# Optimization experiments

Hardware: AMD Instinct MI355X
Metric: run time of the kernel (lower is better)

The kernel has to match this reference:

```python
import jax, jax.numpy as jnp
import numpy as np

L, D, H, KS, VS, HID = 2048, 1024, 16, 1024, 1024, 4096
EPS = 1e-5


def _linear_params(key, din, dout):
    # torch nn.Linear default init: U(-1/sqrt(din), 1/sqrt(din))
    s = 1.0 / np.sqrt(din)
    kw, kb = jax.random.split(key)
    W = jax.random.uniform(kw, (dout, din), minval=-s, maxval=s, dtype=jnp.float32)
    b = jax.random.uniform(kb, (dout,), minval=-s, maxval=s, dtype=jnp.float32)
    return W, b


def setup_inputs() -> dict:
    key = jax.random.key(0)
    ks = jax.random.split(key, 12)
    x = jax.random.normal(ks[0], (L, D), dtype=jnp.float32)
    # inverse shortest-path lengths in [0, 1]
    shortest_path = jax.random.uniform(ks[1], (L, L), dtype=jnp.float32)
    Wq, bq = _linear_params(ks[2], D, KS)
    Wk, bk = _linear_params(ks[3], D, KS)
    Wv, bv = _linear_params(ks[4], D, VS)
    Wqp, bqp = _linear_params(ks[5], KS, KS)
    Wkp, bkp = _linear_params(ks[6], KS, KS)
    Wvp, bvp = _linear_params(ks[7], VS, VS)
    Wo, bo = _linear_params(ks[8], VS, D)
    W1, b1 = _linear_params(ks[9], D, HID)
    W2, b2 = _linear_params(ks[10], HID, D)
    g1 = jnp.ones((D,), jnp.float32); be1 = jnp.zeros((D,), jnp.float32)
    g2 = jnp.ones((D,), jnp.float32); be2 = jnp.zeros((D,), jnp.float32)
    return dict(x=x, shortest_path=shortest_path,
                Wq=Wq, bq=bq, Wk=Wk, bk=bk, Wv=Wv, bv=bv,
                Wqp=Wqp, bqp=bqp, Wkp=Wkp, bkp=bkp, Wvp=Wvp, bvp=bvp,
                Wo=Wo, bo=bo, W1=W1, b1=b1, W2=W2, b2=b2,
                g1=g1, be1=be1, g2=g2, be2=be2)


def _dense(h, W, b):
    return h @ W.T + b


def _layernorm(h, g, b):
    mu = jnp.mean(h, axis=-1, keepdims=True)
    var = jnp.mean(jnp.square(h - mu), axis=-1, keepdims=True)
    return (h - mu) * jax.lax.rsqrt(var + EPS) * g + b


def reference(x, shortest_path, Wq, bq, Wk, bk, Wv, bv, Wqp, bqp, Wkp, bkp,
              Wvp, bvp, Wo, bo, W1, b1, W2, b2, g1, be1, g2, be2):
    hd = KS // H
    vhd = VS // H
    q = _dense(_dense(x, Wq, bq), Wqp, bqp).reshape(L, H, hd).transpose(1, 0, 2)   # [H,L,hd]
    k = _dense(_dense(x, Wk, bk), Wkp, bkp).reshape(L, H, hd).transpose(1, 0, 2)   # [H,L,hd]
    v = _dense(_dense(x, Wv, bv), Wvp, bvp).reshape(L, H, vhd).transpose(1, 0, 2)  # [H,L,vhd]
    att = jnp.einsum('hld,hmd->hlm', q, k) / jnp.sqrt(jnp.float32(hd))             # [H,L,L]
    sp_bias = jax.nn.softmax(shortest_path, axis=-1) * 0.5                          # [L,L]
    att = jax.nn.softmax(att + sp_bias[None, :, :], axis=-1)
    o = jnp.einsum('hlm,hmd->hld', att, v).transpose(1, 0, 2).reshape(L, VS)        # [L,VS]
    o = _dense(o, Wo, bo)
    h = _layernorm(x + o, g1, be1)                # residual + LN1 (dropout=identity)
    f = jax.nn.relu(_dense(jax.nn.relu(_dense(h, W1, b1)), W2, b2))
    return _layernorm(h + f, g2, be2)             # residual + LN2
```

## Files before the change

### kernel.cpp

```cpp
#include <hip/hip_runtime.h>

typedef __attribute__((ext_vector_type(4))) float f32x4;
typedef __attribute__((ext_vector_type(8))) short s16x8;

static __device__ __forceinline__ ushort f2b(float f) {
  union { float f; unsigned u; } v; v.f = f;
  unsigned u = v.u;
  unsigned r = (u + 0x7fffu + ((u >> 16) & 1u)) >> 16;
  return (ushort)r;
}
static __device__ __forceinline__ float b2f(ushort h) {
  union { unsigned u; float f; } v; v.u = ((unsigned)h) << 16;
  return v.f;
}

static __device__ __forceinline__ void gload_lds16(const ushort* g, ushort* l) {
  __builtin_amdgcn_global_load_lds(
      (const __attribute__((address_space(1))) void*)g,
      (__attribute__((address_space(3))) void*)l, 16, 0, 0);
}

struct Cvt7 {
  const float* src[7];
  ushort* dst[7];
  int n[7];
};
__global__ __launch_bounds__(256) void cvt_multi_k(Cvt7 a) {
  int e = blockIdx.y;
  int i = (blockIdx.x * 256 + threadIdx.x) * 4;
  if (i >= a.n[e]) return;
  float4 v4 = *(const float4*)(a.src[e] + i);
  ushort4 o4; o4.x = f2b(v4.x); o4.y = f2b(v4.y); o4.z = f2b(v4.z); o4.w = f2b(v4.w);
  *(ushort4*)(a.dst[e] + i) = o4;
}

__global__ __launch_bounds__(256) void wtr_k(const float* __restrict__ Wq,
                                             const float* __restrict__ Wk,
                                             const float* __restrict__ Wv,
                                             ushort* __restrict__ dst) {
  __shared__ float t[64][65];
  int z = blockIdx.z;
  const float* src = z == 0 ? Wq : (z == 1 ? Wk : Wv);
  float scale = z == 0 ? 0.125f : 1.f;
  int r0 = blockIdx.x * 64, c0 = blockIdx.y * 64;
  int lr = threadIdx.x >> 2, lc4 = (threadIdx.x & 3) * 16;
#pragma unroll
  for (int j = 0; j < 4; ++j)
    *(float4*)&t[lr][lc4 + j * 4] = *(const float4*)(src + (size_t)(r0 + lr) * 1024 + c0 + lc4 + j * 4);
  __syncthreads();
  ushort tmp[16];
#pragma unroll
  for (int j = 0; j < 16; ++j) tmp[j] = f2b(t[lc4 + j][lr] * scale);
  ushort* d = dst + (size_t)z * 1048576 + (size_t)(c0 + lr) * 1024 + r0 + lc4;
  *(uint4*)d = *(uint4*)tmp;
  *(uint4*)(d + 8) = *(uint4*)(tmp + 8);
}

__global__ __launch_bounds__(256) void bvec_k(
    const float* __restrict__ Wqp, const float* __restrict__ Wkp, const float* __restrict__ Wvp,
    const float* __restrict__ bq, const float* __restrict__ bqp,
    const float* __restrict__ bk, const float* __restrict__ bkp,
    const float* __restrict__ bv, const float* __restrict__ bvp,
    float* __restrict__ outb) {
  int r = blockIdx.x * 4 + (threadIdx.x >> 6);
  int lane = threadIdx.x & 63;
  int z = r >> 10, rr = r & 1023;
  const float* Wp = z == 0 ? Wqp : (z == 1 ? Wkp : Wvp);
  const float* bi = z == 0 ? bq : (z == 1 ? bk : bv);
  const float* bp = z == 0 ? bqp : (z == 1 ? bkp : bvp);
  float s = 0.f;
#pragma unroll
  for (int t = 0; t < 4; ++t) {
    float4 w = *(const float4*)(Wp + (size_t)rr * 1024 + lane * 16 + t * 4);
    float4 b = *(const float4*)(bi + lane * 16 + t * 4);
    s += w.x * b.x + w.y * b.y + w.z * b.z + w.w * b.w;
  }
#pragma unroll
  for (int m = 1; m < 64; m <<= 1) s += __shfl_xor(s, m);
  if (lane == 0) outb[r] = (s + bp[rr]) * (z == 0 ? 0.125f : 1.f);
}

__global__ __launch_bounds__(256) void spsm_k(const float* __restrict__ sp,
                                              ushort* __restrict__ out) {
  const int Lc = 2048;
  int row = blockIdx.x;
  int tid = threadIdx.x;
  const float* r = sp + (size_t)row * Lc;
  float v[8];
  float mx = -1e30f;
#pragma unroll
  for (int j = 0; j < 8; ++j) { v[j] = r[tid + j * 256]; mx = fmaxf(mx, v[j]); }
#pragma unroll
  for (int m = 1; m < 64; m <<= 1) mx = fmaxf(mx, __shfl_xor(mx, m));
  __shared__ float redm[4], reds[4];
  if ((tid & 63) == 0) redm[tid >> 6] = mx;
  __syncthreads();
  mx = fmaxf(fmaxf(redm[0], redm[1]), fmaxf(redm[2], redm[3]));
  float s = 0.f;
#pragma unroll
  for (int j = 0; j < 8; ++j) { v[j] = __expf(v[j] - mx); s += v[j]; }
#pragma unroll
  for (int m = 1; m < 64; m <<= 1) s += __shfl_xor(s, m);
  if ((tid & 63) == 0) reds[tid >> 6] = s;
  __syncthreads();
  s = reds[0] + reds[1] + reds[2] + reds[3];
  float inv = 0.5f / s;
  ushort* o = out + (size_t)row * Lc;
#pragma unroll
  for (int j = 0; j < 8; ++j) o[tid + j * 256] = f2b(v[j] * inv);
}

__global__ __launch_bounds__(256) void vtr_k(const ushort* __restrict__ qkv,
                                             ushort* __restrict__ vT) {
  __shared__ ushort t[64][72];
  int tid = threadIdx.x;
  int r = tid >> 3, c8 = (tid & 7) * 8;
  int l0 = blockIdx.x * 64, h = blockIdx.y;
#pragma unroll
  for (int p = 0; p < 2; ++p)
    *(uint4*)&t[r + p * 32][c8] =
        *(const uint4*)(qkv + (size_t)(l0 + r + p * 32) * 3072 + 2048 + h * 64 + c8);
  __syncthreads();
#pragma unroll
  for (int p = 0; p < 2; ++p) {
    int d = r + p * 32;
    ushort tmp[8];
#pragma unroll
    for (int j = 0; j < 8; ++j) tmp[j] = t[c8 + j][d];
    *(uint4*)(vT + ((size_t)h * 64 + d) * 2048 + l0 + c8) = *(uint4*)tmp;
  }
}

template <int BM, int ZM>
__global__ __launch_bounds__(256, 2) void gemm_k(
    const ushort* __restrict__ A, const ushort* __restrict__ W,
    const float* __restrict__ bias, void* __restrict__ Cv,
    int M, int N, int K, int relu, float oscale) {
  constexpr int MT = BM / 32;
  __shared__ ushort As[BM][64];
  __shared__ ushort Bs[128][64];
  const int z = (ZM != 0) ? blockIdx.z : 0;
  if (ZM == 1) { A += (size_t)z * M * K; W += (size_t)z * N * K; }
  int kb0 = 0, kb1 = K;
  if (ZM == 2) { int kh = K >> 1; kb0 = z * kh; kb1 = kb0 + kh; }
  const int tid = threadIdx.x;
  const int lane = tid & 63;
  const int wave = tid >> 6;
  const int wm = (wave >> 1) * (BM / 2);
  const int wn = (wave & 1) * 64;
  const int bm = blockIdx.x * BM;
  const int bn = blockIdx.y * 128;
  const int cl = lane & 15, rg = lane >> 4;
  const int lrow = lane >> 3, lcol = (lane & 7) * 8;

  f32x4 acc[MT][4];
#pragma unroll
  for (int i = 0; i < MT; ++i)
#pragma unroll
    for (int j = 0; j < 4; ++j) acc[i][j] = (f32x4){0.f, 0.f, 0.f, 0.f};

  const ushort* gA = A + (size_t)(bm + wave * 8 + lrow) * K + lcol;
  const ushort* gB = W + (size_t)(bn + wave * 8 + lrow) * K + lcol;
  ushort* lA = &As[wave * 8][0];
  ushort* lB = &Bs[wave * 8][0];

  for (int k0 = kb0; k0 < kb1; k0 += 64) {
#pragma unroll
    for (int c = 0; c < MT; ++c)
      gload_lds16(gA + (size_t)(c * 32) * K + k0, lA + c * 2048);
#pragma unroll
    for (int c = 0; c < 4; ++c)
      gload_lds16(gB + (size_t)(c * 32) * K + k0, lB + c * 2048);
    __syncthreads();
    const int kbo = 8 * rg;
#pragma unroll
    for (int kk = 0; kk < 64; kk += 32) {
      s16x8 af[MT], bf[4];
#pragma unroll
      for (int mt = 0; mt < MT; ++mt)
        af[mt] = *(const s16x8*)&As[wm + mt * 16 + cl][kk + kbo];
#pragma unroll
      for (int nt = 0; nt < 4; ++nt)
        bf[nt] = *(const s16x8*)&Bs[wn + nt * 16 + cl][kk + kbo];
#pragma unroll
      for (int mt = 0; mt < MT; ++mt)
#pragma unroll
        for (int nt = 0; nt < 4; ++nt)
          acc[mt][nt] = __builtin_amdgcn_mfma_f32_16x16x32_bf16(af[mt], bf[nt], acc[mt][nt], 0, 0, 0);
    }
    __syncthreads();
  }

  if (ZM == 2) {
    float* Cf = (float*)Cv + (size_t)z * M * N;
#pragma unroll
    for (int nt = 0; nt < 4; ++nt) {
      int c = bn + wn + nt * 16 + cl;
#pragma unroll
      for (int mt = 0; mt < MT; ++mt)
#pragma unroll
        for (int i = 0; i < 4; ++i) {
          int r = bm + wm + mt * 16 + rg * 4 + i;
          Cf[(size_t)r * N + c] = acc[mt][nt][i];
        }
    }
  } else {
    ushort* Cu = (ushort*)Cv;
    if (ZM == 1) Cu += (size_t)z * M * N;
#pragma unroll
    for (int nt = 0; nt < 4; ++nt) {
      int c = bn + wn + nt * 16 + cl;
      float bv = bias ? bias[c] : 0.f;
#pragma unroll
      for (int mt = 0; mt < MT; ++mt) {
#pragma unroll
        for (int i = 0; i < 4; ++i) {
          int r = bm + wm + mt * 16 + rg * 4 + i;
          float v = (acc[mt][nt][i] + bv) * oscale;
          if (relu) v = fmaxf(v, 0.f);
          Cu[(size_t)r * N + c] = f2b(v);
        }
      }
    }
  }
}

__global__ __launch_bounds__(256) void comb2_k(const float* __restrict__ p,
                                               const float* __restrict__ bias,
                                               ushort* __restrict__ out, int relu) {
  const int MN = 2048 * 1024;
  int i = (blockIdx.x * 256 + threadIdx.x) * 4;
  float4 a = *(const float4*)(p + i);
  float4 b = *(const float4*)(p + MN + i);
  float4 bb = *(const float4*)(bias + (i & 1023));
  float v0 = a.x + b.x + bb.x, v1 = a.y + b.y + bb.y;
  float v2 = a.z + b.z + bb.z, v3 = a.w + b.w + bb.w;
  if (relu) {
    v0 = fmaxf(v0, 0.f); v1 = fmaxf(v1, 0.f);
    v2 = fmaxf(v2, 0.f); v3 = fmaxf(v3, 0.f);
  }
  ushort4 o; o.x = f2b(v0); o.y = f2b(v1); o.z = f2b(v2); o.w = f2b(v3);
  *(ushort4*)(out + i) = o;
}

__global__ __launch_bounds__(256, 2) void attn_k(
    const ushort* __restrict__ qkv, const ushort* __restrict__ vT,
    const ushort* __restrict__ biasb, ushort* __restrict__ opart,
    float* __restrict__ lbuf) {
  const int Lc = 2048;
  int h = blockIdx.x;
  int m0 = blockIdx.y * 64;
  int s = blockIdx.z;
  int nb = s * 1024, ne = nb + 1024;
  int tid = threadIdx.x, lane = tid & 63, wave = tid >> 6;

  __shared__ ushort Qs[64][72];
  __shared__ ushort Ks[64][72];
  __shared__ ushort Vs[64][72];
  __shared__ ushort Ps[4][16][72];

  int srow = tid >> 3, scol = (tid & 7) * 8;
#pragma unroll
  for (int p = 0; p < 2; ++p) {
    int r = srow + p * 32;
    *(uint4*)&Qs[r][scol] = *(const uint4*)(qkv + (size_t)(m0 + r) * 3072 + h * 64 + scol);
  }

  f32x4 oacc[4];
#pragma unroll
  for (int i = 0; i < 4; ++i) oacc[i] = (f32x4){0.f, 0.f, 0.f, 0.f};
  float lacc[4] = {0.f, 0.f, 0.f, 0.f};

  const int rg = lane >> 4, cl = lane & 15;
  const int kb = 8 * rg;

  for (int n0 = nb; n0 < ne; n0 += 64) {
    __syncthreads();
#pragma unroll
    for (int p = 0; p < 2; ++p) {
      int r = srow + p * 32;
      *(uint4*)&Ks[r][scol] = *(const uint4*)(qkv + (size_t)(n0 + r) * 3072 + 1024 + h * 64 + scol);
      *(uint4*)&Vs[r][scol] = *(const uint4*)(vT + ((size_t)h * 64 + r) * 2048 + n0 + scol);
    }
    __syncthreads();

    f32x4 sacc[4];
#pragma unroll
    for (int nt = 0; nt < 4; ++nt)
#pragma unroll
      for (int i = 0; i < 4; ++i)
        sacc[nt][i] =
            b2f(biasb[(size_t)(m0 + wave * 16 + rg * 4 + i) * Lc + n0 + nt * 16 + cl]) - 8.f;

#pragma unroll
    for (int kk = 0; kk < 64; kk += 32) {
      s16x8 a = *(const s16x8*)&Qs[wave * 16 + cl][kk + kb];
#pragma unroll
      for (int nt = 0; nt < 4; ++nt) {
        s16x8 b = *(const s16x8*)&Ks[nt * 16 + cl][kk + kb];
        sacc[nt] = __builtin_amdgcn_mfma_f32_16x16x32_bf16(a, b, sacc[nt], 0, 0, 0);
      }
    }
#pragma unroll
    for (int i = 0; i < 4; ++i) {
#pragma unroll
      for (int nt = 0; nt < 4; ++nt) {
        float pv = __expf(sacc[nt][i]);
        sacc[nt][i] = pv;
        lacc[i] += pv;
      }
    }
#pragma unroll
    for (int nt = 0; nt < 4; ++nt)
#pragma unroll
      for (int i = 0; i < 4; ++i)
        Ps[wave][rg * 4 + i][nt * 16 + cl] = f2b(sacc[nt][i]);
#pragma unroll
    for (int kk = 0; kk < 64; kk += 32) {
      s16x8 a = *(const s16x8*)&Ps[wave][cl][kk + kb];
#pragma unroll
      for (int nt = 0; nt < 4; ++nt) {
        s16x8 b = *(const s16x8*)&Vs[nt * 16 + cl][kk + kb];
        oacc[nt] = __builtin_amdgcn_mfma_f32_16x16x32_bf16(a, b, oacc[nt], 0, 0, 0);
      }
    }
  }
#pragma unroll
  for (int nt = 0; nt < 4; ++nt) {
#pragma unroll
    for (int i = 0; i < 4; ++i) {
      int r = m0 + wave * 16 + rg * 4 + i;
      opart[((size_t)s * Lc + r) * 1024 + h * 64 + nt * 16 + cl] = f2b(oacc[nt][i]);
    }
  }
#pragma unroll
  for (int i = 0; i < 4; ++i) {
    float l = lacc[i];
#pragma unroll
    for (int m = 1; m < 16; m <<= 1) l += __shfl_xor(l, m);
    if (cl == 0) {
      int r = m0 + wave * 16 + rg * 4 + i;
      lbuf[(size_t)(s * 16 + h) * Lc + r] = l;
    }
  }
}

__global__ __launch_bounds__(256) void acomb_k(const ushort* __restrict__ op,
                                               const float* __restrict__ lbuf,
                                               ushort* __restrict__ ob) {
  const int Lc = 2048;
  int qrow = blockIdx.x;
  int tid = threadIdx.x;
  int c = tid * 4;
  int h = c >> 6;
  float l0 = lbuf[(size_t)h * Lc + qrow];
  float l1 = lbuf[(size_t)(16 + h) * Lc + qrow];
  float inv = 1.f / (l0 + l1);
  ushort4 a = *(const ushort4*)(op + (size_t)qrow * 1024 + c);
  ushort4 b = *(const ushort4*)(op + ((size_t)Lc + qrow) * 1024 + c);
  ushort4 o;
  o.x = f2b((b2f(a.x) + b2f(b.x)) * inv);
  o.y = f2b((b2f(a.y) + b2f(b.y)) * inv);
  o.z = f2b((b2f(a.z) + b2f(b.z)) * inv);
  o.w = f2b((b2f(a.w) + b2f(b.w)) * inv);
  *(ushort4*)(ob + (size_t)qrow * 1024 + c) = o;
}

__global__ __launch_bounds__(256) void ln_k(const float* __restrict__ base,
                                            const ushort* __restrict__ add,
                                            const float* __restrict__ g,
                                            const float* __restrict__ be,
                                            ushort* __restrict__ outb,
                                            float* __restrict__ outf) {
  const int Dc = 1024;
  int row = blockIdx.x;
  int tid = threadIdx.x;
  float4 bx = *(const float4*)(base + (size_t)row * Dc + tid * 4);
  ushort4 ax = *(const ushort4*)(add + (size_t)row * Dc + tid * 4);
  float v0 = bx.x + b2f(ax.x), v1 = bx.y + b2f(ax.y);
  float v2 = bx.z + b2f(ax.z), v3 = bx.w + b2f(ax.w);
  float s = v0 + v1 + v2 + v3;
  __shared__ float red[4];
#pragma unroll
  for (int m = 1; m < 64; m <<= 1) s += __shfl_xor(s, m);
  if ((tid & 63) == 0) red[tid >> 6] = s;
  __syncthreads();
  s = red[0] + red[1] + red[2] + red[3];
  float mu = s * (1.f / Dc);
  float d0 = v0 - mu, d1 = v1 - mu, d2 = v2 - mu, d3 = v3 - mu;
  float ss = d0 * d0 + d1 * d1 + d2 * d2 + d3 * d3;
  __syncthreads();
#pragma unroll
  for (int m = 1; m < 64; m <<= 1) ss += __shfl_xor(ss, m);
  if ((tid & 63) == 0) red[tid >> 6] = ss;
  __syncthreads();
  ss = red[0] + red[1] + red[2] + red[3];
  float rs = rsqrtf(ss * (1.f / Dc) + 1e-5f);
  int c = tid * 4;
  float4 gv = *(const float4*)(g + c);
  float4 bev = *(const float4*)(be + c);
  float y0 = d0 * rs * gv.x + bev.x;
  float y1 = d1 * rs * gv.y + bev.y;
  float y2 = d2 * rs * gv.z + bev.z;
  float y3 = d3 * rs * gv.w + bev.w;
  size_t o = (size_t)row * Dc + c;
  if (outb) {
    ushort4 ob4; ob4.x = f2b(y0); ob4.y = f2b(y1); ob4.z = f2b(y2); ob4.w = f2b(y3);
    *(ushort4*)(outb + o) = ob4;
  }
  if (outf) {
    float4 of4; of4.x = y0; of4.y = y1; of4.z = y2; of4.w = y3;
    *(float4*)(outf + o) = of4;
  }
}

extern "C" void kernel_launch(void* const* d_in, const int* in_sizes, int n_in,
                              void* d_out, int out_size, void* d_ws, size_t ws_size,
                              hipStream_t stream) {
  const int L = 2048, D = 1024, H = 16, HID = 4096;
  const float* x   = (const float*)d_in[0];
  const float* sp  = (const float*)d_in[1];
  const float* Wq  = (const float*)d_in[2];  const float* bq  = (const float*)d_in[3];
  const float* Wk  = (const float*)d_in[4];  const float* bk  = (const float*)d_in[5];
  const float* Wv  = (const float*)d_in[6];  const float* bv  = (const float*)d_in[7];
  const float* Wqp = (const float*)d_in[8];  const float* bqp = (const float*)d_in[9];
  const float* Wkp = (const float*)d_in[10]; const float* bkp = (const float*)d_in[11];
  const float* Wvp = (const float*)d_in[12]; const float* bvp = (const float*)d_in[13];
  const float* Wo  = (const float*)d_in[14]; const float* bo  = (const float*)d_in[15];
  const float* W1  = (const float*)d_in[16]; const float* b1  = (const float*)d_in[17];
  const float* W2  = (const float*)d_in[18]; const float* b2  = (const float*)d_in[19];
  const float* g1  = (const float*)d_in[20]; const float* be1 = (const float*)d_in[21];
  const float* g2  = (const float*)d_in[22]; const float* be2 = (const float*)d_in[23];
  float* out = (float*)d_out;

  size_t off = 0;
  char* base = (char*)d_ws;
  auto alloc = [&](size_t b) {
    char* p = base + off;
    off += (b + 255) & ~(size_t)255;
    return p;
  };
  ushort* xb    = (ushort*)alloc((size_t)L * D * 2);
  ushort* wqpb  = (ushort*)alloc((size_t)D * D * 2);
  ushort* wkpb  = (ushort*)alloc((size_t)D * D * 2);
  ushort* wvpb  = (ushort*)alloc((size_t)D * D * 2);
  ushort* wqTb  = (ushort*)alloc((size_t)3 * D * D * 2);
  ushort* wfused= (ushort*)alloc((size_t)3 * D * D * 2);
  ushort* qkv   = (ushort*)alloc((size_t)L * 3072 * 2);
  float*  bfused= (float*)alloc((size_t)3072 * 4);
  ushort* wob   = (ushort*)alloc((size_t)D * D * 2);
  ushort* w1b   = (ushort*)alloc((size_t)HID * D * 2);
  ushort* w2b   = (ushort*)alloc((size_t)D * HID * 2);
  ushort* spsb  = (ushort*)alloc((size_t)L * L * 2);
  ushort* opart = (ushort*)alloc((size_t)2 * L * 1024 * 2);
  ushort* vT    = (ushort*)alloc((size_t)H * 64 * L * 2);
  float*  lbuf  = (float*)alloc((size_t)2 * H * L * 4);
  ushort* ob    = (ushort*)alloc((size_t)L * 1024 * 2);
  ushort* hb    = (ushort*)alloc((size_t)L * D * 2);
  float*  hf    = (float*)alloc((size_t)L * D * 4);

  ushort* ffn1  = wqTb;
  float*  parts = (float*)spsb;
  ushort* opb   = vT;
  ushort* fb    = ob;

  Cvt7 ca;
  ca.src[0] = x;   ca.dst[0] = xb;   ca.n[0] = L * D;
  ca.src[1] = Wqp; ca.dst[1] = wqpb; ca.n[1] = D * D;
  ca.src[2] = Wkp; ca.dst[2] = wkpb; ca.n[2] = D * D;
  ca.src[3] = Wvp; ca.dst[3] = wvpb; ca.n[3] = D * D;
  ca.src[4] = Wo;  ca.dst[4] = wob;  ca.n[4] = D * D;
  ca.src[5] = W1;  ca.dst[5] = w1b;  ca.n[5] = HID * D;
  ca.src[6] = W2;  ca.dst[6] = w2b;  ca.n[6] = D * HID;
  cvt_multi_k<<<dim3(4096, 7), dim3(256), 0, stream>>>(ca);

  wtr_k<<<dim3(16, 16, 3), dim3(256), 0, stream>>>(Wq, Wk, Wv, wqTb);
  bvec_k<<<dim3(768), dim3(256), 0, stream>>>(Wqp, Wkp, Wvp, bq, bqp, bk, bkp, bv, bvp, bfused);
  spsm_k<<<dim3(L), dim3(256), 0, stream>>>(sp, spsb);

  gemm_k<64, 1><<<dim3(16, 8, 3), dim3(256), 0, stream>>>(
      wqpb, wqTb, (const float*)nullptr, wfused, D, D, D, 0, 1.f);
  gemm_k<64, 0><<<dim3(32, 24), dim3(256), 0, stream>>>(
      xb, wfused, bfused, qkv, L, 3072, D, 0, 1.f);

  vtr_k<<<dim3(L / 64, H), dim3(256), 0, stream>>>(qkv, vT);
  attn_k<<<dim3(H, L / 64, 2), dim3(256), 0, stream>>>(qkv, vT, spsb, opart, lbuf);
  acomb_k<<<dim3(L), dim3(256), 0, stream>>>(opart, lbuf, ob);

  gemm_k<64, 2><<<dim3(32, 8, 2), dim3(256), 0, stream>>>(
      ob, wob, (const float*)nullptr, parts, L, D, D, 0, 1.f);
  comb2_k<<<dim3(2048), dim3(256), 0, stream>>>(parts, bo, opb, 0);
  ln_k<<<dim3(L), dim3(256), 0, stream>>>(x, opb, g1, be1, hb, hf);
  gemm_k<128, 0><<<dim3(16, 32), dim3(256), 0, stream>>>(
      hb, w1b, b1, ffn1, L, HID, D, 1, 1.f);
  gemm_k<64, 2><<<dim3(32, 8, 2), dim3(256), 0, stream>>>(
      ffn1, w2b, (const float*)nullptr, parts, L, D, HID, 0, 1.f);
  comb2_k<<<dim3(2048), dim3(256), 0, stream>>>(parts, b2, fb, 1);
  ln_k<<<dim3(L), dim3(256), 0, stream>>>(hf, fb, g2, be2, (ushort*)nullptr, out);
}
```

Measured before the change: 227.7 us.

## Double-buffer GEMM LDS, prefetch attention tiles, fuse split-K combine into layernorm

The GEMM now double-buffers its LDS tiles so the next K-tile's global-to-LDS load overlaps the MFMA work on the current one. The attention kernel keeps Q in registers, prefetches the K, V and bias tiles into registers one iteration ahead, stages the bias through LDS, raises wave priority around the MFMA blocks, and remaps block IDs with XCD-aware swizzling. Separate comb2 kernels are removed by having the layernorm sum the two split-K partials, add the bias, apply relu and add the residual. Packed bf16 conversion replaces the scalar rounding. The changes add register and LDS pressure (double LDS in the GEMM, higher occupancy target in attention). The GEMM loop also assumes an even number of K tiles.

Result: slower. 287.7 us (+26.3%).

```diff
diff --git a/kernel.cpp b/kernel.cpp
--- a/kernel.cpp
+++ b/kernel.cpp
@@ -12,6 +12,11 @@
 static __device__ __forceinline__ float b2f(ushort h) {
   union { unsigned u; float f; } v; v.u = ((unsigned)h) << 16;
   return v.f;
+}
+static __device__ __forceinline__ unsigned cvtpk(float a, float b) {
+  unsigned r;
+  asm("v_cvt_pk_bf16_f32 %0, %1, %2" : "=v"(r) : "v"(a), "v"(b));
+  return r;
 }
 
 static __device__ __forceinline__ void gload_lds16(const ushort* g, ushort* l) {
@@ -137,8 +142,8 @@
     const float* __restrict__ bias, void* __restrict__ Cv,
     int M, int N, int K, int relu, float oscale) {
   constexpr int MT = BM / 32;
-  __shared__ ushort As[BM][64];
-  __shared__ ushort Bs[128][64];
+  __shared__ ushort As0[BM][64], Bs0[128][64];
+  __shared__ ushort As1[BM][64], Bs1[128][64];
   const int z = (ZM != 0) ? blockIdx.z : 0;
   if (ZM == 1) { A += (size_t)z * M * K; W += (size_t)z * N * K; }
   int kb0 = 0, kb1 = K;
@@ -161,33 +166,43 @@
 
   const ushort* gA = A + (size_t)(bm + wave * 8 + lrow) * K + lcol;
   const ushort* gB = W + (size_t)(bn + wave * 8 + lrow) * K + lcol;
-  ushort* lA = &As[wave * 8][0];
-  ushort* lB = &Bs[wave * 8][0];
-
-  for (int k0 = kb0; k0 < kb1; k0 += 64) {
+
+  auto stage = [&](ushort* lA, ushort* lB, int k0) {
 #pragma unroll
     for (int c = 0; c < MT; ++c)
-      gload_lds16(gA + (size_t)(c * 32) * K + k0, lA + c * 2048);
+      gload_lds16(gA + (size_t)(c * 32) * K + k0, lA + wave * 512 + c * 2048);
 #pragma unroll
     for (int c = 0; c < 4; ++c)
-      gload_lds16(gB + (size_t)(c * 32) * K + k0, lB + c * 2048);
-    __syncthreads();
+      gload_lds16(gB + (size_t)(c * 32) * K + k0, lB + wave * 512 + c * 2048);
+  };
+  auto compute = [&](const ushort* As, const ushort* Bs) {
     const int kbo = 8 * rg;
 #pragma unroll
     for (int kk = 0; kk < 64; kk += 32) {
       s16x8 af[MT], bf[4];
 #pragma unroll
       for (int mt = 0; mt < MT; ++mt)
-        af[mt] = *(const s16x8*)&As[wm + mt * 16 + cl][kk + kbo];
+        af[mt] = *(const s16x8*)(As + (wm + mt * 16 + cl) * 64 + kk + kbo);
 #pragma unroll
       for (int nt = 0; nt < 4; ++nt)
-        bf[nt] = *(const s16x8*)&Bs[wn + nt * 16 + cl][kk + kbo];
+        bf[nt] = *(const s16x8*)(Bs + (wn + nt * 16 + cl) * 64 + kk + kbo);
 #pragma unroll
       for (int mt = 0; mt < MT; ++mt)
 #pragma unroll
         for (int nt = 0; nt < 4; ++nt)
           acc[mt][nt] = __builtin_amdgcn_mfma_f32_16x16x32_bf16(af[mt], bf[nt], acc[mt][nt], 0, 0, 0);
     }
+  };
+
+  const int ktiles = (kb1 - kb0) >> 6;
+  stage(&As0[0][0], &Bs0[0][0], kb0);
+  __syncthreads();
+  for (int tt = 0; tt < ktiles; tt += 2) {
+    stage(&As1[0][0], &Bs1[0][0], kb0 + (tt + 1) * 64);
+    compute(&As0[0][0], &Bs0[0][0]);
+    __syncthreads();
+    if (tt + 2 < ktiles) stage(&As0[0][0], &Bs0[0][0], kb0 + (tt + 2) * 64);
+    compute(&As1[0][0], &Bs1[0][0]);
     __syncthreads();
   }
 
@@ -213,94 +228,100 @@
       float bv = bias ? bias[c] : 0.f;
 #pragma unroll
       for (int mt = 0; mt < MT; ++mt) {
-#pragma unroll
-        for (int i = 0; i < 4; ++i) {
-          int r = bm + wm + mt * 16 + rg * 4 + i;
-          float v = (acc[mt][nt][i] + bv) * oscale;
-          if (relu) v = fmaxf(v, 0.f);
-          Cu[(size_t)r * N + c] = f2b(v);
+        float v0 = (acc[mt][nt][0] + bv) * oscale;
+        float v1 = (acc[mt][nt][1] + bv) * oscale;
+        float v2 = (acc[mt][nt][2] + bv) * oscale;
+        float v3 = (acc[mt][nt][3] + bv) * oscale;
+        if (relu) {
+          v0 = fmaxf(v0, 0.f); v1 = fmaxf(v1, 0.f);
+          v2 = fmaxf(v2, 0.f); v3 = fmaxf(v3, 0.f);
         }
+        unsigned p01 = cvtpk(v0, v1), p23 = cvtpk(v2, v3);
+        size_t b = (size_t)(bm + wm + mt * 16 + rg * 4) * N + c;
+        Cu[b] = (ushort)p01;
+        Cu[b + N] = (ushort)(p01 >> 16);
+        Cu[b + 2 * N] = (ushort)p23;
+        Cu[b + 3 * N] = (ushort)(p23 >> 16);
       }
     }
   }
 }
 
-__global__ __launch_bounds__(256) void comb2_k(const float* __restrict__ p,
-                                               const float* __restrict__ bias,
-                                               ushort* __restrict__ out, int relu) {
-  const int MN = 2048 * 1024;
-  int i = (blockIdx.x * 256 + threadIdx.x) * 4;
-  float4 a = *(const float4*)(p + i);
-  float4 b = *(const float4*)(p + MN + i);
-  float4 bb = *(const float4*)(bias + (i & 1023));
-  float v0 = a.x + b.x + bb.x, v1 = a.y + b.y + bb.y;
-  float v2 = a.z + b.z + bb.z, v3 = a.w + b.w + bb.w;
-  if (relu) {
-    v0 = fmaxf(v0, 0.f); v1 = fmaxf(v1, 0.f);
-    v2 = fmaxf(v2, 0.f); v3 = fmaxf(v3, 0.f);
-  }
-  ushort4 o; o.x = f2b(v0); o.y = f2b(v1); o.z = f2b(v2); o.w = f2b(v3);
-  *(ushort4*)(out + i) = o;
-}
-
-__global__ __launch_bounds__(256, 2) void attn_k(
+__global__ __launch_bounds__(256, 4) void attn_k(
     const ushort* __restrict__ qkv, const ushort* __restrict__ vT,
     const ushort* __restrict__ biasb, ushort* __restrict__ opart,
     float* __restrict__ lbuf) {
   const int Lc = 2048;
-  int h = blockIdx.x;
-  int m0 = blockIdx.y * 64;
-  int s = blockIdx.z;
+  int bid = blockIdx.x;
+  int xcd = bid & 7, t = bid >> 3;
+  int h = t & 15;
+  int p = ((t >> 4) << 3) | xcd;
+  int m0 = (p & 31) * 64;
+  int s = p >> 5;
   int nb = s * 1024, ne = nb + 1024;
   int tid = threadIdx.x, lane = tid & 63, wave = tid >> 6;
 
-  __shared__ ushort Qs[64][72];
   __shared__ ushort Ks[64][72];
   __shared__ ushort Vs[64][72];
   __shared__ ushort Ps[4][16][72];
-
+  __shared__ ushort Bs2[64][72];
+
+  const int rg = lane >> 4, cl = lane & 15;
+  const int kb = 8 * rg;
   int srow = tid >> 3, scol = (tid & 7) * 8;
-#pragma unroll
-  for (int p = 0; p < 2; ++p) {
-    int r = srow + p * 32;
-    *(uint4*)&Qs[r][scol] = *(const uint4*)(qkv + (size_t)(m0 + r) * 3072 + h * 64 + scol);
-  }
+
+  const ushort* qp = qkv + (size_t)(m0 + wave * 16 + cl) * 3072 + h * 64;
+  s16x8 qfr[2];
+  qfr[0] = *(const s16x8*)(qp + kb);
+  qfr[1] = *(const s16x8*)(qp + 32 + kb);
 
   f32x4 oacc[4];
 #pragma unroll
   for (int i = 0; i < 4; ++i) oacc[i] = (f32x4){0.f, 0.f, 0.f, 0.f};
   float lacc[4] = {0.f, 0.f, 0.f, 0.f};
 
-  const int rg = lane >> 4, cl = lane & 15;
-  const int kb = 8 * rg;
-
+  uint4 kreg[2], vreg[2], breg[2];
+  auto loadtile = [&](int n0) {
+#pragma unroll
+    for (int pp = 0; pp < 2; ++pp) {
+      int r = srow + pp * 32;
+      kreg[pp] = *(const uint4*)(qkv + (size_t)(n0 + r) * 3072 + 1024 + h * 64 + scol);
+      vreg[pp] = *(const uint4*)(vT + ((size_t)h * 64 + r) * 2048 + n0 + scol);
+      breg[pp] = *(const uint4*)(biasb + (size_t)(m0 + r) * Lc + n0 + scol);
+    }
+  };
+
+  loadtile(nb);
   for (int n0 = nb; n0 < ne; n0 += 64) {
     __syncthreads();
 #pragma unroll
-    for (int p = 0; p < 2; ++p) {
-      int r = srow + p * 32;
-      *(uint4*)&Ks[r][scol] = *(const uint4*)(qkv + (size_t)(n0 + r) * 3072 + 1024 + h * 64 + scol);
-      *(uint4*)&Vs[r][scol] = *(const uint4*)(vT + ((size_t)h * 64 + r) * 2048 + n0 + scol);
+    for (int pp = 0; pp < 2; ++pp) {
+      int r = srow + pp * 32;
+      *(uint4*)&Ks[r][scol] = kreg[pp];
+      *(uint4*)&Vs[r][scol] = vreg[pp];
+      *(uint4*)&Bs2[r][scol] = breg[pp];
     }
     __syncthreads();
+    if (n0 + 64 < ne) loadtile(n0 + 64);
 
     f32x4 sacc[4];
 #pragma unroll
     for (int nt = 0; nt < 4; ++nt)
 #pragma unroll
       for (int i = 0; i < 4; ++i)
-        sacc[nt][i] =
-            b2f(biasb[(size_t)(m0 + wave * 16 + rg * 4 + i) * Lc + n0 + nt * 16 + cl]) - 8.f;
-
-#pragma unroll
-    for (int kk = 0; kk < 64; kk += 32) {
-      s16x8 a = *(const s16x8*)&Qs[wave * 16 + cl][kk + kb];
+        sacc[nt][i] = b2f(Bs2[wave * 16 + rg * 4 + i][nt * 16 + cl]) - 8.f;
+
+    __builtin_amdgcn_s_setprio(1);
+#pragma unroll
+    for (int kk2 = 0; kk2 < 2; ++kk2) {
 #pragma unroll
       for (int nt = 0; nt < 4; ++nt) {
-        s16x8 b = *(const s16x8*)&Ks[nt * 16 + cl][kk + kb];
-        sacc[nt] = __builtin_amdgcn_mfma_f32_16x16x32_bf16(a, b, sacc[nt], 0, 0, 0);
+        s16x8 b = *(const s16x8*)&Ks[nt * 16 + cl][kk2 * 32 + kb];
+        sacc[nt] = __builtin_amdgcn_mfma_f32_16x16x32_bf16(qfr[kk2], b, sacc[nt], 0, 0, 0);
       }
     }
+    __builtin_amdgcn_s_setprio(0);
+
 #pragma unroll
     for (int i = 0; i < 4; ++i) {
 #pragma unroll
@@ -311,10 +332,15 @@
       }
     }
 #pragma unroll
-    for (int nt = 0; nt < 4; ++nt)
-#pragma unroll
-      for (int i = 0; i < 4; ++i)
-        Ps[wave][rg * 4 + i][nt * 16 + cl] = f2b(sacc[nt][i]);
+    for (int nt = 0; nt < 4; ++nt) {
+      unsigned p01 = cvtpk(sacc[nt][0], sacc[nt][1]);
+      unsigned p23 = cvtpk(sacc[nt][2], sacc[nt][3]);
+      Ps[wave][rg * 4 + 0][nt * 16 + cl] = (ushort)p01;
+      Ps[wave][rg * 4 + 1][nt * 16 + cl] = (ushort)(p01 >> 16);
+      Ps[wave][rg * 4 + 2][nt * 16 + cl] = (ushort)p23;
+      Ps[wave][rg * 4 + 3][nt * 16 + cl] = (ushort)(p23 >> 16);
+    }
+    __builtin_amdgcn_s_setprio(1);
 #pragma unroll
     for (int kk = 0; kk < 64; kk += 32) {
       s16x8 a = *(const s16x8*)&Ps[wave][cl][kk + kb];
@@ -324,14 +350,17 @@
         oacc[nt] = __builtin_amdgcn_mfma_f32_16x16x32_bf16(a, b, oacc[nt], 0, 0, 0);
       }
     }
+    __builtin_amdgcn_s_setprio(0);
   }
 #pragma unroll
   for (int nt = 0; nt < 4; ++nt) {
-#pragma unroll
-    for (int i = 0; i < 4; ++i) {
-      int r = m0 + wave * 16 + rg * 4 + i;
-      opart[((size_t)s * Lc + r) * 1024 + h * 64 + nt * 16 + cl] = f2b(oacc[nt][i]);
-    }
+    unsigned p01 = cvtpk(oacc[nt][0], oacc[nt][1]);
+    unsigned p23 = cvtpk(oacc[nt][2], oacc[nt][3]);
+    size_t b = ((size_t)s * Lc + (m0 + wave * 16 + rg * 4)) * 1024 + h * 64 + nt * 16 + cl;
+    opart[b] = (ushort)p01;
+    opart[b + 1024] = (ushort)(p01 >> 16);
+    opart[b + 2048] = (ushort)p23;
+    opart[b + 3072] = (ushort)(p23 >> 16);
   }
 #pragma unroll
   for (int i = 0; i < 4; ++i) {
@@ -366,19 +395,30 @@
   *(ushort4*)(ob + (size_t)qrow * 1024 + c) = o;
 }
 
-__global__ __launch_bounds__(256) void ln_k(const float* __restrict__ base,
-                                            const ushort* __restrict__ add,
-                                            const float* __restrict__ g,
-                                            const float* __restrict__ be,
-                                            ushort* __restrict__ outb,
-                                            float* __restrict__ outf) {
+__global__ __launch_bounds__(256) void lnf_k(const float* __restrict__ basef,
+                                             const float* __restrict__ p,
+                                             const float* __restrict__ bvec,
+                                             const float* __restrict__ g,
+                                             const float* __restrict__ be,
+                                             int relu,
+                                             ushort* __restrict__ outb,
+                                             float* __restrict__ outf) {
   const int Dc = 1024;
+  const size_t MN = (size_t)2048 * 1024;
   int row = blockIdx.x;
   int tid = threadIdx.x;
-  float4 bx = *(const float4*)(base + (size_t)row * Dc + tid * 4);
-  ushort4 ax = *(const ushort4*)(add + (size_t)row * Dc + tid * 4);
-  float v0 = bx.x + b2f(ax.x), v1 = bx.y + b2f(ax.y);
-  float v2 = bx.z + b2f(ax.z), v3 = bx.w + b2f(ax.w);
+  int c = tid * 4;
+  float4 bx = *(const float4*)(basef + (size_t)row * Dc + c);
+  float4 a0 = *(const float4*)(p + (size_t)row * Dc + c);
+  float4 a1 = *(const float4*)(p + MN + (size_t)row * Dc + c);
+  float4 bb = *(const float4*)(bvec + c);
+  float v0 = a0.x + a1.x + bb.x, v1 = a0.y + a1.y + bb.y;
+  float v2 = a0.z + a1.z + bb.z, v3 = a0.w + a1.w + bb.w;
+  if (relu) {
+    v0 = fmaxf(v0, 0.f); v1 = fmaxf(v1, 0.f);
+    v2 = fmaxf(v2, 0.f); v3 = fmaxf(v3, 0.f);
+  }
+  v0 += bx.x; v1 += bx.y; v2 += bx.z; v3 += bx.w;
   float s = v0 + v1 + v2 + v3;
   __shared__ float red[4];
 #pragma unroll
@@ -396,7 +436,6 @@
   __syncthreads();
   ss = red[0] + red[1] + red[2] + red[3];
   float rs = rsqrtf(ss * (1.f / Dc) + 1e-5f);
-  int c = tid * 4;
   float4 gv = *(const float4*)(g + c);
   float4 bev = *(const float4*)(be + c);
   float y0 = d0 * rs * gv.x + bev.x;
@@ -461,8 +500,6 @@
 
   ushort* ffn1  = wqTb;
   float*  parts = (float*)spsb;
-  ushort* opb   = vT;
-  ushort* fb    = ob;
 
   Cvt7 ca;
   ca.src[0] = x;   ca.dst[0] = xb;   ca.n[0] = L * D;
@@ -484,17 +521,15 @@
       xb, wfused, bfused, qkv, L, 3072, D, 0, 1.f);
 
   vtr_k<<<dim3(L / 64, H), dim3(256), 0, stream>>>(qkv, vT);
-  attn_k<<<dim3(H, L / 64, 2), dim3(256), 0, stream>>>(qkv, vT, spsb, opart, lbuf);
+  attn_k<<<dim3(H * (L / 64) * 2), dim3(256), 0, stream>>>(qkv, vT, spsb, opart, lbuf);
   acomb_k<<<dim3(L), dim3(256), 0, stream>>>(opart, lbuf, ob);
 
   gemm_k<64, 2><<<dim3(32, 8, 2), dim3(256), 0, stream>>>(
       ob, wob, (const float*)nullptr, parts, L, D, D, 0, 1.f);
-  comb2_k<<<dim3(2048), dim3(256), 0, stream>>>(parts, bo, opb, 0);
-  ln_k<<<dim3(L), dim3(256), 0, stream>>>(x, opb, g1, be1, hb, hf);
+  lnf_k<<<dim3(L), dim3(256), 0, stream>>>(x, parts, bo, g1, be1, 0, hb, hf);
   gemm_k<128, 0><<<dim3(16, 32), dim3(256), 0, stream>>>(
       hb, w1b, b1, ffn1, L, HID, D, 1, 1.f);
   gemm_k<64, 2><<<dim3(32, 8, 2), dim3(256), 0, stream>>>(
       ffn1, w2b, (const float*)nullptr, parts, L, D, HID, 0, 1.f);
-  comb2_k<<<dim3(2048), dim3(256), 0, stream>>>(parts, b2, fb, 1);
-  ln_k<<<dim3(L), dim3(256), 0, stream>>>(hf, fb, g2, be2, (ushort*)nullptr, out);
-}
+  lnf_k<<<dim3(L), dim3(256), 0, stream>>>(hf, parts, b2, g2, be2, 1, (ushort*)nullptr, out);
+}
```
